# Kernel optimization log

Measured on AMD Instinct MI355X. Metric: run time of the kernel, lower is better.

The kernel has to match this reference:

```python
import jax, jax.numpy as jnp
import numpy as np

TEMPERATURE = 0.07
IGNORE_INDEX = -100
NEG_INF = -1e30


def setup_inputs() -> dict:
    key = jax.random.key(0)
    kg, ke, kl = jax.random.split(key, 3)
    B, P, H = 4, 4096, 256
    greek_embeds = jax.random.normal(kg, (B, P, H), dtype=jnp.float32)
    english_embeds = jax.random.normal(ke, (B, P, H), dtype=jnp.float32)
    # labels in {1 aligned, 0 not aligned, -100 ignore}, ~1/3 each
    raw = jax.random.randint(kl, (B, P), 0, 3)
    labels = jnp.where(raw == 2, IGNORE_INDEX, raw).astype(jnp.int32)
    return {"greek_embeds": greek_embeds, "english_embeds": english_embeds, "labels": labels}


def reference(greek_embeds, english_embeds, labels):
    # L2-normalize (F.normalize semantics: clamp norm at 1e-12)
    g = greek_embeds / jnp.clip(jnp.linalg.norm(greek_embeds, axis=-1, keepdims=True), 1e-12)
    e = english_embeds / jnp.clip(jnp.linalg.norm(english_embeds, axis=-1, keepdims=True), 1e-12)
    # [B, P, P] similarity
    sim = jnp.einsum("bph,bqh->bpq", g, e) / TEMPERATURE

    valid = labels != IGNORE_INDEX            # [B, P]
    pos = valid & (labels == 1)               # [B, P]
    neg = valid & (labels != 1)               # [B, P]
    # batch is processed only if >=2 valid pairs AND at least one pos AND one neg
    batch_ok = (valid.sum(-1) >= 2) & pos.any(-1) & neg.any(-1)  # [B]

    diag = jnp.diagonal(sim, axis1=1, axis2=2)                   # [B, P] positive logit
    neg_sims = jnp.where(neg[:, None, :], sim, NEG_INF)          # [B, P, P] negative logits
    # stable logsumexp over concat([diag_i], neg_sims_i)
    m = jnp.maximum(diag, neg_sims.max(-1))                      # [B, P]
    lse = m + jnp.log(jnp.exp(diag - m) + jnp.sum(jnp.exp(neg_sims - m[..., None]), -1))
    per_pos_loss = lse - diag                                    # cross_entropy with target=0

    mask = pos & batch_ok[:, None]
    count = mask.sum()
    total = jnp.sum(jnp.where(mask, per_pos_loss, 0.0))
    return jnp.where(count == 0, 0.0, total / count.astype(total.dtype))
```

## Files before the change

kernel.cpp:

```cpp
#include <hip/hip_runtime.h>
#include <hip/hip_bf16.h>
#include <math.h>

#define BB 4
#define PP 4096
#define HH 256
#define INV_T (1.0f/0.07f)
#define JSPLIT 8
#define NTILES (PP/16)
#define TILE_BYTES (16*HH*2)

typedef __attribute__((ext_vector_type(8))) short bf16x8;
typedef __attribute__((ext_vector_type(4))) float f32x4;

#define WAITVM(n) asm volatile("s_waitcnt vmcnt(" #n ")" ::: "memory")

__device__ __forceinline__ float waveReduceSum(float v){
  #pragma unroll
  for (int off = 32; off; off >>= 1) v += __shfl_xor(v, off);
  return v;
}

__device__ __forceinline__ unsigned short f2bf(float x){
  union { float f; unsigned u; } v; v.f = x;
  unsigned r = v.u + 0x7FFFu + ((v.u >> 16) & 1u);
  return (unsigned short)(r >> 16);
}

__device__ __forceinline__ void gload_lds16(const void* g, void* l){
  __builtin_amdgcn_global_load_lds(
      (const __attribute__((address_space(1))) unsigned int*)g,
      (__attribute__((address_space(3))) unsigned int*)l, 16, 0, 0);
}

__global__ void k_compact(const int* __restrict__ labels, int* __restrict__ meta,
                          int* __restrict__ posIdx, int* __restrict__ negIdx){
  int b = blockIdx.x;
  const int* lab = labels + b * PP;
  __shared__ int wP[4], wN[4], wV[4];
  __shared__ int basePos, baseNeg, baseVal;
  int tid = threadIdx.x, wave = tid >> 6, lane = tid & 63;
  if (tid == 0){ basePos = 0; baseNeg = 0; baseVal = 0; }
  __syncthreads();
  for (int c = 0; c < PP; c += 256){
    int p = c + tid;
    int l = lab[p];
    bool isP = (l == 1), isN = (l == 0), isV = (l != -100);
    unsigned long long bP = __ballot(isP), bN = __ballot(isN), bV = __ballot(isV);
    unsigned long long lt = (1ull << lane) - 1ull;
    if (lane == 0){ wP[wave] = __popcll(bP); wN[wave] = __popcll(bN); wV[wave] = __popcll(bV); }
    __syncthreads();
    int offP = 0, offN = 0;
    for (int w = 0; w < wave; w++){ offP += wP[w]; offN += wN[w]; }
    if (isP) posIdx[b*PP + basePos + offP + __popcll(bP & lt)] = p;
    if (isN) negIdx[b*PP + baseNeg + offN + __popcll(bN & lt)] = p;
    __syncthreads();
    if (tid == 0){
      basePos += wP[0] + wP[1] + wP[2] + wP[3];
      baseNeg += wN[0] + wN[1] + wN[2] + wN[3];
      baseVal += wV[0] + wV[1] + wV[2] + wV[3];
    }
    __syncthreads();
  }
  if (tid == 0){
    int Np = basePos, Nn = baseNeg, nv = baseVal;
    meta[b*4+0] = Np;
    meta[b*4+1] = Nn;
    meta[b*4+2] = (nv >= 2 && Np > 0 && Nn > 0) ? 1 : 0;
    meta[b*4+3] = nv;
  }
}

__global__ void k_norm(const float* __restrict__ greek, const float* __restrict__ english,
                       const int* __restrict__ meta, const int* __restrict__ posIdx,
                       const int* __restrict__ negIdx,
                       unsigned short* __restrict__ GposF, unsigned short* __restrict__ EnegF,
                       float* __restrict__ diag){
  int tid = threadIdx.x, wave = tid >> 6, lane = tid & 63;
  int gb = blockIdx.x;
  const int HALF = BB * PP / 4;
  bool isPos = gb < HALF;
  int rowBase = (gb % HALF) * 4 + wave;
  int b = rowBase / PP;
  int i = rowBase % PP;
  int Np = meta[b*4+0], Nn = meta[b*4+1];
  int Ncount = isPos ? Np : Nn;
  unsigned short* buf = isPos ? GposF : EnegF;
  char* dst = (char*)buf + ((size_t)b*NTILES + (i>>4))*TILE_BYTES
            + (lane>>3)*1024 + (((i&15) + ((lane>>1)&3)*16) << 4);

  if (i >= Ncount){
    if (i < ((Ncount + 15) & ~15) && !(lane & 1))
      *(uint4*)dst = make_uint4(0u,0u,0u,0u);
    return;
  }
  const int* idx = isPos ? posIdx : negIdx;
  int p = idx[b*PP + i];
  size_t base = ((size_t)b * PP + p) * HH + lane * 4;

  if (isPos){
    float4 g4 = *reinterpret_cast<const float4*>(greek + base);
    float ssg = waveReduceSum(g4.x*g4.x + g4.y*g4.y + g4.z*g4.z + g4.w*g4.w);
    float gs = 1.0f / fmaxf(sqrtf(ssg), 1e-12f);
    float gx = g4.x*gs, gy = g4.y*gs, gz = g4.z*gs, gw = g4.w*gs;
    unsigned u0 = (unsigned)f2bf(gx) | ((unsigned)f2bf(gy) << 16);
    unsigned u1 = (unsigned)f2bf(gz) | ((unsigned)f2bf(gw) << 16);
    unsigned o0 = __shfl_xor(u0, 1), o1 = __shfl_xor(u1, 1);
    if (!(lane & 1)) *(uint4*)dst = make_uint4(u0, u1, o0, o1);
    float4 e4 = *reinterpret_cast<const float4*>(english + base);
    float sse = waveReduceSum(e4.x*e4.x + e4.y*e4.y + e4.z*e4.z + e4.w*e4.w);
    float es = 1.0f / fmaxf(sqrtf(sse), 1e-12f);
    float d = waveReduceSum((gx*e4.x + gy*e4.y + gz*e4.z + gw*e4.w) * es);
    if (lane == 0) diag[b*PP + i] = d;
  } else {
    float4 e4 = *reinterpret_cast<const float4*>(english + base);
    float sse = waveReduceSum(e4.x*e4.x + e4.y*e4.y + e4.z*e4.z + e4.w*e4.w);
    float es = 1.0f / fmaxf(sqrtf(sse), 1e-12f);
    unsigned u0 = (unsigned)f2bf(e4.x*es) | ((unsigned)f2bf(e4.y*es) << 16);
    unsigned u1 = (unsigned)f2bf(e4.z*es) | ((unsigned)f2bf(e4.w*es) << 16);
    unsigned o0 = __shfl_xor(u0, 1), o1 = __shfl_xor(u1, 1);
    if (!(lane & 1)) *(uint4*)dst = make_uint4(u0, u1, o0, o1);
  }
}

__global__ void __launch_bounds__(256, 4)
k_loss(const unsigned short* __restrict__ GposF,
       const unsigned short* __restrict__ EnegF,
       const int* __restrict__ meta,
       float* __restrict__ Spart){
  int L = blockIdx.x;
  int rb = L >> 5;
  int pair = L & 31;
  int b = pair >> 3, chunk = pair & 7;
  int Np = meta[b*4+0], Nn = meta[b*4+1], ok = meta[b*4+2];
  int i0 = rb * 64;
  if (!ok || i0 >= Np) return;
  int tid = threadIdx.x, wave = tid >> 6, lane = tid & 63;
  int lo16 = lane & 15, hi4 = lane >> 4;
  int NT = (Nn + 15) >> 4;
  int TPC = (NT + JSPLIT - 1) / JSPLIT;
  int t0 = chunk * TPC, t1 = min(NT, t0 + TPC);

  __shared__ __align__(16) char Bs[3][TILE_BYTES];

  const char* AF = (const char*)GposF + ((size_t)b*NTILES + (i0 >> 4) + wave) * TILE_BYTES;
  bf16x8 a[8];
  #pragma unroll
  for (int kk = 0; kk < 8; kk++)
    a[kk] = *reinterpret_cast<const bf16x8*>(AF + kk*1024 + (lane << 4));

  const char* EF = (const char*)EnegF + (size_t)b * NTILES * TILE_BYTES;
  float s[4] = {0.f, 0.f, 0.f, 0.f};

  if (t0 < t1){
    {
      const char* src = EF + (size_t)t0*TILE_BYTES + (wave << 11) + (lane << 4);
      char* dstl = &Bs[0][wave << 11];
      gload_lds16(src, dstl);
      gload_lds16(src + 1024, dstl + 1024);
    }
    if (t0 + 1 < t1){
      const char* src = EF + (size_t)(t0+1)*TILE_BYTES + (wave << 11) + (lane << 4);
      char* dstl = &Bs[1][wave << 11];
      gload_lds16(src, dstl);
      gload_lds16(src + 1024, dstl + 1024);
    }
    int cur = 0;
    for (int t = t0; t < t1; t++){
      if (t + 1 < t1) WAITVM(2);
      else            WAITVM(0);
      __builtin_amdgcn_s_barrier();
      __builtin_amdgcn_sched_barrier(0);

      if (t + 2 < t1){
        int nb = cur + 2; if (nb >= 3) nb -= 3;
        const char* src = EF + (size_t)(t+2)*TILE_BYTES + (wave << 11) + (lane << 4);
        char* dstl = &Bs[nb][wave << 11];
        gload_lds16(src, dstl);
        gload_lds16(src + 1024, dstl + 1024);
      }

      const char* Bt = &Bs[cur][0];
      f32x4 c = {0.f, 0.f, 0.f, 0.f};
      #pragma unroll
      for (int kk = 0; kk < 8; kk++){
        bf16x8 bv = *reinterpret_cast<const bf16x8*>(Bt + kk*1024 + (lane << 4));
        c = __builtin_amdgcn_mfma_f32_16x16x32_bf16(a[kk], bv, c, 0, 0, 0);
      }
      bool cok = (t*16 + lo16) < Nn;
      #pragma unroll
      for (int r = 0; r < 4; r++)
        s[r] += cok ? __expf(c[r] * INV_T) : 0.0f;

      cur = (cur == 2) ? 0 : cur + 1;
    }
  }

  #pragma unroll
  for (int off = 1; off < 16; off <<= 1){
    #pragma unroll
    for (int r = 0; r < 4; r++) s[r] += __shfl_xor(s[r], off);
  }
  if (lo16 == 0){
    #pragma unroll
    for (int r = 0; r < 4; r++){
      int i = i0 + wave*16 + hi4*4 + r;
      Spart[(((size_t)b*PP + i) << 3) + chunk] = s[r];
    }
  }
}

__global__ void k_final(const float* __restrict__ Spart, const float* __restrict__ diag,
                        const int* __restrict__ meta, float* __restrict__ out){
  __shared__ float lds[16];
  int tid = threadIdx.x;
  int np[BB], okk[BB];
  #pragma unroll
  for (int b = 0; b < BB; b++){ np[b] = meta[b*4+0]; okk[b] = meta[b*4+2]; }
  float tot = 0.0f;
  for (int idx = tid; idx < BB*PP; idx += 1024){
    int b = idx >> 12, i = idx & (PP-1);
    if (!okk[b] || i >= np[b]) continue;
    const float4* p = reinterpret_cast<const float4*>(Spart + ((size_t)idx << 3));
    float4 p0 = p[0], p1 = p[1];
    float S = ((p0.x+p0.y)+(p0.z+p0.w)) + ((p1.x+p1.y)+(p1.z+p1.w));
    float dl = diag[idx] * INV_T;
    tot += logf(S + expf(dl)) - dl;
  }
  #pragma unroll
  for (int off = 32; off; off >>= 1) tot += __shfl_xor(tot, off);
  int wave = tid >> 6;
  if ((tid & 63) == 0) lds[wave] = tot;
  __syncthreads();
  if (tid == 0){
    float total = 0.0f;
    #pragma unroll
    for (int w = 0; w < 16; w++) total += lds[w];
    int count = 0;
    #pragma unroll
    for (int b = 0; b < BB; b++) if (okk[b]) count += np[b];
    out[0] = (count == 0) ? 0.0f : total / (float)count;
  }
}

extern "C" void kernel_launch(void* const* d_in, const int* in_sizes, int n_in,
                              void* d_out, int out_size, void* d_ws, size_t ws_size,
                              hipStream_t stream){
  const float* greek   = (const float*)d_in[0];
  const float* english = (const float*)d_in[1];
  const int*   labels  = (const int*)d_in[2];
  float* out = (float*)d_out;

  char* ws = (char*)d_ws;
  size_t off = 0;
  unsigned short* GposF = (unsigned short*)(ws + off); off += (size_t)BB*NTILES*TILE_BYTES;
  unsigned short* EnegF = (unsigned short*)(ws + off); off += (size_t)BB*NTILES*TILE_BYTES;
  float* Spart  = (float*)(ws + off); off += (size_t)BB*PP*JSPLIT*sizeof(float);
  float* diag   = (float*)(ws + off); off += (size_t)BB*PP*sizeof(float);
  int*   posIdx = (int*)(ws + off);   off += (size_t)BB*PP*sizeof(int);
  int*   negIdx = (int*)(ws + off);   off += (size_t)BB*PP*sizeof(int);
  int*   meta   = (int*)(ws + off);   off += 64;

  k_compact<<<BB, 256, 0, stream>>>(labels, meta, posIdx, negIdx);
  k_norm<<<2*BB*PP/4, 256, 0, stream>>>(greek, english, meta, posIdx, negIdx,
                                        GposF, EnegF, diag);
  k_loss<<<(PP/64)*32, 256, 0, stream>>>(GposF, EnegF, meta, Spart);
  k_final<<<1, 1024, 0, stream>>>(Spart, diag, meta, out);
}
```

Before: 42.19 us.

## Fuse prep kernels, mask negatives by bitmask, and fold final reduction into loss kernel

Merges label compaction and normalization into one prep kernel. Normalized rows are now written in natural row order instead of being gathered into compacted MFMA tiles. The loss kernel no longer works on a compacted negative set: it sweeps all columns and masks non-negatives with a per-batch bitmask. It then finishes the per-row logsumexp and the global mean with last-block atomic counters, which removes the separate final kernel. This cuts launches and the serial compaction-to-normalize dependency, but roughly triples the matmul and exp work in the loss kernel and adds atomics and fences.

```diff
diff --git a/kernel.cpp b/kernel.cpp
--- a/kernel.cpp
+++ b/kernel.cpp
@@ -6,20 +6,15 @@
 #define PP 4096
 #define HH 256
 #define INV_T (1.0f/0.07f)
-#define JSPLIT 8
-#define NTILES (PP/16)
-#define TILE_BYTES (16*HH*2)
+#define NRB 64
+#define TPC 32
+#define TILE_BYTES 8192
+#define D2GRID (NRB*32)
 
 typedef __attribute__((ext_vector_type(8))) short bf16x8;
 typedef __attribute__((ext_vector_type(4))) float f32x4;
 
 #define WAITVM(n) asm volatile("s_waitcnt vmcnt(" #n ")" ::: "memory")
-
-__device__ __forceinline__ float waveReduceSum(float v){
-  #pragma unroll
-  for (int off = 32; off; off >>= 1) v += __shfl_xor(v, off);
-  return v;
-}
 
 __device__ __forceinline__ unsigned short f2bf(float x){
   union { float f; unsigned u; } v; v.f = x;
@@ -33,213 +28,211 @@
       (__attribute__((address_space(3))) unsigned int*)l, 16, 0, 0);
 }
 
-__global__ void k_compact(const int* __restrict__ labels, int* __restrict__ meta,
-                          int* __restrict__ posIdx, int* __restrict__ negIdx){
-  int b = blockIdx.x;
-  const int* lab = labels + b * PP;
-  __shared__ int wP[4], wN[4], wV[4];
-  __shared__ int basePos, baseNeg, baseVal;
+__global__ void k_prep(const float* __restrict__ greek, const float* __restrict__ english,
+                       const int* __restrict__ labels,
+                       unsigned short* __restrict__ Gn, unsigned short* __restrict__ En,
+                       float* __restrict__ diagN, int* __restrict__ posIdx,
+                       int* __restrict__ meta, unsigned* __restrict__ negBits,
+                       int* __restrict__ ctrRB, float* __restrict__ partialTot,
+                       int* __restrict__ gctr){
   int tid = threadIdx.x, wave = tid >> 6, lane = tid & 63;
-  if (tid == 0){ basePos = 0; baseNeg = 0; baseVal = 0; }
-  __syncthreads();
-  for (int c = 0; c < PP; c += 256){
-    int p = c + tid;
-    int l = lab[p];
-    bool isP = (l == 1), isN = (l == 0), isV = (l != -100);
-    unsigned long long bP = __ballot(isP), bN = __ballot(isN), bV = __ballot(isV);
-    unsigned long long lt = (1ull << lane) - 1ull;
-    if (lane == 0){ wP[wave] = __popcll(bP); wN[wave] = __popcll(bN); wV[wave] = __popcll(bV); }
-    __syncthreads();
-    int offP = 0, offN = 0;
-    for (int w = 0; w < wave; w++){ offP += wP[w]; offN += wN[w]; }
-    if (isP) posIdx[b*PP + basePos + offP + __popcll(bP & lt)] = p;
-    if (isN) negIdx[b*PP + baseNeg + offN + __popcll(bN & lt)] = p;
-    __syncthreads();
+  if (blockIdx.x < BB){
+    int b = blockIdx.x;
+    if (tid < NRB){ ctrRB[b*NRB + tid] = 0; partialTot[b*NRB + tid] = 0.0f; }
+    if (b == 0 && tid == 64) gctr[0] = 0;
+    const int* lab = labels + b * PP;
+    __shared__ int wP[4], wN[4], wV[4];
+    __shared__ int basePos, baseNeg, baseVal;
+    if (tid == 0){ basePos = 0; baseNeg = 0; baseVal = 0; }
+    __syncthreads();
+    for (int c = 0; c < PP; c += 256){
+      int p = c + tid;
+      int l = lab[p];
+      bool isP = (l == 1), isN = (l == 0), isV = (l != -100);
+      unsigned long long bP = __ballot(isP), bN = __ballot(isN), bV = __ballot(isV);
+      unsigned long long lt = (1ull << lane) - 1ull;
+      if (lane == 0){
+        wP[wave] = __popcll(bP); wN[wave] = __popcll(bN); wV[wave] = __popcll(bV);
+        int w0 = (c + (wave << 6)) >> 5;
+        negBits[b*128 + w0]     = (unsigned)bN;
+        negBits[b*128 + w0 + 1] = (unsigned)(bN >> 32);
+      }
+      __syncthreads();
+      int offP = 0;
+      for (int w = 0; w < wave; w++) offP += wP[w];
+      if (isP) posIdx[b*PP + basePos + offP + __popcll(bP & lt)] = p;
+      __syncthreads();
+      if (tid == 0){
+        basePos += wP[0]+wP[1]+wP[2]+wP[3];
+        baseNeg += wN[0]+wN[1]+wN[2]+wN[3];
+        baseVal += wV[0]+wV[1]+wV[2]+wV[3];
+      }
+      __syncthreads();
+    }
     if (tid == 0){
-      basePos += wP[0] + wP[1] + wP[2] + wP[3];
-      baseNeg += wN[0] + wN[1] + wN[2] + wN[3];
-      baseVal += wV[0] + wV[1] + wV[2] + wV[3];
-    }
-    __syncthreads();
+      int Np = basePos, Nn = baseNeg, nv = baseVal;
+      meta[b*4+0] = Np; meta[b*4+1] = Nn;
+      meta[b*4+2] = (nv >= 2 && Np > 0 && Nn > 0) ? 1 : 0;
+      meta[b*4+3] = nv;
+    }
+  } else {
+    int u = (blockIdx.x - BB) * 4 + wave;
+    int lab = labels[u];
+    if (lab == -100) return;
+    size_t base = (size_t)u * HH + lane * 4;
+    if (lab == 1){
+      float4 g4 = *reinterpret_cast<const float4*>(greek + base);
+      float4 e4 = *reinterpret_cast<const float4*>(english + base);
+      float ag = g4.x*g4.x + g4.y*g4.y + g4.z*g4.z + g4.w*g4.w;
+      float ae = e4.x*e4.x + e4.y*e4.y + e4.z*e4.z + e4.w*e4.w;
+      float ad = g4.x*e4.x + g4.y*e4.y + g4.z*e4.z + g4.w*e4.w;
+      #pragma unroll
+      for (int off = 32; off; off >>= 1){
+        ag += __shfl_xor(ag, off); ae += __shfl_xor(ae, off); ad += __shfl_xor(ad, off);
+      }
+      float gs = 1.0f / fmaxf(sqrtf(ag), 1e-12f);
+      float es = 1.0f / fmaxf(sqrtf(ae), 1e-12f);
+      ushort4 go; go.x=f2bf(g4.x*gs); go.y=f2bf(g4.y*gs); go.z=f2bf(g4.z*gs); go.w=f2bf(g4.w*gs);
+      *reinterpret_cast<ushort4*>(Gn + (size_t)u*HH + lane*4) = go;
+      if (lane == 0) diagN[u] = ad * gs * es;
+    } else {
+      float4 e4 = *reinterpret_cast<const float4*>(english + base);
+      float ae = e4.x*e4.x + e4.y*e4.y + e4.z*e4.z + e4.w*e4.w;
+      #pragma unroll
+      for (int off = 32; off; off >>= 1) ae += __shfl_xor(ae, off);
+      float es = 1.0f / fmaxf(sqrtf(ae), 1e-12f);
+      ushort4 eo; eo.x=f2bf(e4.x*es); eo.y=f2bf(e4.y*es); eo.z=f2bf(e4.z*es); eo.w=f2bf(e4.w*es);
+      *reinterpret_cast<ushort4*>(En + (size_t)u*HH + lane*4) = eo;
+    }
   }
-  if (tid == 0){
-    int Np = basePos, Nn = baseNeg, nv = baseVal;
-    meta[b*4+0] = Np;
-    meta[b*4+1] = Nn;
-    meta[b*4+2] = (nv >= 2 && Np > 0 && Nn > 0) ? 1 : 0;
-    meta[b*4+3] = nv;
-  }
-}
-
-__global__ void k_norm(const float* __restrict__ greek, const float* __restrict__ english,
-                       const int* __restrict__ meta, const int* __restrict__ posIdx,
-                       const int* __restrict__ negIdx,
-                       unsigned short* __restrict__ GposF, unsigned short* __restrict__ EnegF,
-                       float* __restrict__ diag){
-  int tid = threadIdx.x, wave = tid >> 6, lane = tid & 63;
-  int gb = blockIdx.x;
-  const int HALF = BB * PP / 4;
-  bool isPos = gb < HALF;
-  int rowBase = (gb % HALF) * 4 + wave;
-  int b = rowBase / PP;
-  int i = rowBase % PP;
-  int Np = meta[b*4+0], Nn = meta[b*4+1];
-  int Ncount = isPos ? Np : Nn;
-  unsigned short* buf = isPos ? GposF : EnegF;
-  char* dst = (char*)buf + ((size_t)b*NTILES + (i>>4))*TILE_BYTES
-            + (lane>>3)*1024 + (((i&15) + ((lane>>1)&3)*16) << 4);
-
-  if (i >= Ncount){
-    if (i < ((Ncount + 15) & ~15) && !(lane & 1))
-      *(uint4*)dst = make_uint4(0u,0u,0u,0u);
-    return;
-  }
-  const int* idx = isPos ? posIdx : negIdx;
-  int p = idx[b*PP + i];
-  size_t base = ((size_t)b * PP + p) * HH + lane * 4;
-
-  if (isPos){
-    float4 g4 = *reinterpret_cast<const float4*>(greek + base);
-    float ssg = waveReduceSum(g4.x*g4.x + g4.y*g4.y + g4.z*g4.z + g4.w*g4.w);
-    float gs = 1.0f / fmaxf(sqrtf(ssg), 1e-12f);
-    float gx = g4.x*gs, gy = g4.y*gs, gz = g4.z*gs, gw = g4.w*gs;
-    unsigned u0 = (unsigned)f2bf(gx) | ((unsigned)f2bf(gy) << 16);
-    unsigned u1 = (unsigned)f2bf(gz) | ((unsigned)f2bf(gw) << 16);
-    unsigned o0 = __shfl_xor(u0, 1), o1 = __shfl_xor(u1, 1);
-    if (!(lane & 1)) *(uint4*)dst = make_uint4(u0, u1, o0, o1);
-    float4 e4 = *reinterpret_cast<const float4*>(english + base);
-    float sse = waveReduceSum(e4.x*e4.x + e4.y*e4.y + e4.z*e4.z + e4.w*e4.w);
-    float es = 1.0f / fmaxf(sqrtf(sse), 1e-12f);
-    float d = waveReduceSum((gx*e4.x + gy*e4.y + gz*e4.z + gw*e4.w) * es);
-    if (lane == 0) diag[b*PP + i] = d;
-  } else {
-    float4 e4 = *reinterpret_cast<const float4*>(english + base);
-    float sse = waveReduceSum(e4.x*e4.x + e4.y*e4.y + e4.z*e4.z + e4.w*e4.w);
-    float es = 1.0f / fmaxf(sqrtf(sse), 1e-12f);
-    unsigned u0 = (unsigned)f2bf(e4.x*es) | ((unsigned)f2bf(e4.y*es) << 16);
-    unsigned u1 = (unsigned)f2bf(e4.z*es) | ((unsigned)f2bf(e4.w*es) << 16);
-    unsigned o0 = __shfl_xor(u0, 1), o1 = __shfl_xor(u1, 1);
-    if (!(lane & 1)) *(uint4*)dst = make_uint4(u0, u1, o0, o1);
-  }
 }
 
 __global__ void __launch_bounds__(256, 4)
-k_loss(const unsigned short* __restrict__ GposF,
-       const unsigned short* __restrict__ EnegF,
-       const int* __restrict__ meta,
-       float* __restrict__ Spart){
+k_loss(const unsigned short* __restrict__ Gn, const unsigned short* __restrict__ En,
+       const float* __restrict__ diagN, const int* __restrict__ posIdx,
+       const int* __restrict__ meta, const unsigned* __restrict__ negBits,
+       float* __restrict__ Spart, int* __restrict__ ctrRB,
+       float* __restrict__ partialTot, int* __restrict__ gctr,
+       float* __restrict__ out){
   int L = blockIdx.x;
-  int rb = L >> 5;
-  int pair = L & 31;
-  int b = pair >> 3, chunk = pair & 7;
-  int Np = meta[b*4+0], Nn = meta[b*4+1], ok = meta[b*4+2];
-  int i0 = rb * 64;
-  if (!ok || i0 >= Np) return;
+  int rb = L >> 5, b = (L >> 3) & 3, chunk = L & 7;
   int tid = threadIdx.x, wave = tid >> 6, lane = tid & 63;
   int lo16 = lane & 15, hi4 = lane >> 4;
-  int NT = (Nn + 15) >> 4;
-  int TPC = (NT + JSPLIT - 1) / JSPLIT;
-  int t0 = chunk * TPC, t1 = min(NT, t0 + TPC);
+  int Np = meta[b*4+0], ok = meta[b*4+2];
+  int i0 = rb * 64;
+  bool active = ok && (i0 < Np);
 
   __shared__ __align__(16) char Bs[3][TILE_BYTES];
-
-  const char* AF = (const char*)GposF + ((size_t)b*NTILES + (i0 >> 4) + wave) * TILE_BYTES;
-  bf16x8 a[8];
-  #pragma unroll
-  for (int kk = 0; kk < 8; kk++)
-    a[kk] = *reinterpret_cast<const bf16x8*>(AF + kk*1024 + (lane << 4));
-
-  const char* EF = (const char*)EnegF + (size_t)b * NTILES * TILE_BYTES;
-  float s[4] = {0.f, 0.f, 0.f, 0.f};
-
-  if (t0 < t1){
-    {
-      const char* src = EF + (size_t)t0*TILE_BYTES + (wave << 11) + (lane << 4);
-      char* dstl = &Bs[0][wave << 11];
-      gload_lds16(src, dstl);
-      gload_lds16(src + 1024, dstl + 1024);
-    }
-    if (t0 + 1 < t1){
-      const char* src = EF + (size_t)(t0+1)*TILE_BYTES + (wave << 11) + (lane << 4);
-      char* dstl = &Bs[1][wave << 11];
-      gload_lds16(src, dstl);
-      gload_lds16(src + 1024, dstl + 1024);
-    }
+  __shared__ unsigned nb16[16];
+  __shared__ int shI;
+  __shared__ float shF[4];
+
+  if (active){
+    if (tid < 16) nb16[tid] = negBits[b*128 + chunk*16 + tid];
+
+    int iw = i0 + wave*16;
+    int ii = min(iw + lo16, Np-1);
+    int prow = posIdx[b*PP + ii];
+    const char* Ab = (const char*)Gn + ((size_t)b*PP + prow)*(HH*2) + hi4*16;
+    bf16x8 a[8];
+    #pragma unroll
+    for (int kk = 0; kk < 8; kk++)
+      a[kk] = *reinterpret_cast<const bf16x8*>(Ab + kk*64);
+
+    const char* Eb = (const char*)En + (size_t)b*PP*(HH*2);
+    int T0 = chunk * TPC;
+    __syncthreads();
+
+    auto STAGE = [&](int t, int buf){
+      size_t cb = (size_t)(t*16 + lo16)*(HH*2) + hi4*16;
+      char* d = &Bs[buf][wave << 11];
+      gload_lds16(Eb + cb + (size_t)(2*wave+0)*64, d);
+      gload_lds16(Eb + cb + (size_t)(2*wave+1)*64, d + 1024);
+    };
+    STAGE(T0, 0);
+    STAGE(T0+1, 1);
+
+    float s[4] = {0.f,0.f,0.f,0.f};
     int cur = 0;
-    for (int t = t0; t < t1; t++){
-      if (t + 1 < t1) WAITVM(2);
-      else            WAITVM(0);
+    for (int t = T0; t < T0 + TPC; t++){
+      if (t + 1 < T0 + TPC) WAITVM(2);
+      else                  WAITVM(0);
       __builtin_amdgcn_s_barrier();
       __builtin_amdgcn_sched_barrier(0);
-
-      if (t + 2 < t1){
-        int nb = cur + 2; if (nb >= 3) nb -= 3;
-        const char* src = EF + (size_t)(t+2)*TILE_BYTES + (wave << 11) + (lane << 4);
-        char* dstl = &Bs[nb][wave << 11];
-        gload_lds16(src, dstl);
-        gload_lds16(src + 1024, dstl + 1024);
-      }
-
+      if (t + 2 < T0 + TPC){
+        int nbuf = cur + 2; if (nbuf >= 3) nbuf -= 3;
+        STAGE(t+2, nbuf);
+      }
       const char* Bt = &Bs[cur][0];
-      f32x4 c = {0.f, 0.f, 0.f, 0.f};
+      f32x4 c = {0.f,0.f,0.f,0.f};
       #pragma unroll
       for (int kk = 0; kk < 8; kk++){
         bf16x8 bv = *reinterpret_cast<const bf16x8*>(Bt + kk*1024 + (lane << 4));
         c = __builtin_amdgcn_mfma_f32_16x16x32_bf16(a[kk], bv, c, 0, 0, 0);
       }
-      bool cok = (t*16 + lo16) < Nn;
+      unsigned mw = nb16[(t >> 1) - chunk*16];
+      bool cok = (mw >> (lo16 + ((t & 1) << 4))) & 1;
       #pragma unroll
       for (int r = 0; r < 4; r++)
         s[r] += cok ? __expf(c[r] * INV_T) : 0.0f;
-
       cur = (cur == 2) ? 0 : cur + 1;
     }
+
+    #pragma unroll
+    for (int off = 1; off < 16; off <<= 1){
+      #pragma unroll
+      for (int r = 0; r < 4; r++) s[r] += __shfl_xor(s[r], off);
+    }
+    if (lo16 == 0){
+      #pragma unroll
+      for (int r = 0; r < 4; r++){
+        int i = iw + hi4*4 + r;
+        Spart[(((size_t)b*PP + i) << 3) + chunk] = s[r];
+      }
+    }
+
+    __threadfence();
+    if (tid == 0) shI = atomicAdd(&ctrRB[b*NRB + rb], 1);
+    __syncthreads();
+    if (shI == 7){
+      __threadfence();
+      if (tid < 64){
+        float v = 0.0f;
+        int i = i0 + tid;
+        if (i < Np){
+          const float4* p4 = reinterpret_cast<const float4*>(Spart + (((size_t)b*PP + i) << 3));
+          float4 p0 = p4[0], p1 = p4[1];
+          float S = ((p0.x+p0.y)+(p0.z+p0.w)) + ((p1.x+p1.y)+(p1.z+p1.w));
+          float dl = diagN[b*PP + posIdx[b*PP + i]] * INV_T;
+          v = logf(S + __expf(dl)) - dl;
+        }
+        #pragma unroll
+        for (int off = 32; off; off >>= 1) v += __shfl_xor(v, off);
+        if (tid == 0) partialTot[b*NRB + rb] = v;
+      }
+      __threadfence();
+    }
   }
 
-  #pragma unroll
-  for (int off = 1; off < 16; off <<= 1){
+  __syncthreads();
+  if (tid == 0) shI = atomicAdd(gctr, 1);
+  __syncthreads();
+  if (shI == D2GRID - 1){
+    __threadfence();
+    float v = 0.0f;
+    int b2 = tid >> 6;
+    if (meta[b2*4+2]) v = partialTot[tid];
     #pragma unroll
-    for (int r = 0; r < 4; r++) s[r] += __shfl_xor(s[r], off);
-  }
-  if (lo16 == 0){
-    #pragma unroll
-    for (int r = 0; r < 4; r++){
-      int i = i0 + wave*16 + hi4*4 + r;
-      Spart[(((size_t)b*PP + i) << 3) + chunk] = s[r];
-    }
-  }
-}
-
-__global__ void k_final(const float* __restrict__ Spart, const float* __restrict__ diag,
-                        const int* __restrict__ meta, float* __restrict__ out){
-  __shared__ float lds[16];
-  int tid = threadIdx.x;
-  int np[BB], okk[BB];
-  #pragma unroll
-  for (int b = 0; b < BB; b++){ np[b] = meta[b*4+0]; okk[b] = meta[b*4+2]; }
-  float tot = 0.0f;
-  for (int idx = tid; idx < BB*PP; idx += 1024){
-    int b = idx >> 12, i = idx & (PP-1);
-    if (!okk[b] || i >= np[b]) continue;
-    const float4* p = reinterpret_cast<const float4*>(Spart + ((size_t)idx << 3));
-    float4 p0 = p[0], p1 = p[1];
-    float S = ((p0.x+p0.y)+(p0.z+p0.w)) + ((p1.x+p1.y)+(p1.z+p1.w));
-    float dl = diag[idx] * INV_T;
-    tot += logf(S + expf(dl)) - dl;
-  }
-  #pragma unroll
-  for (int off = 32; off; off >>= 1) tot += __shfl_xor(tot, off);
-  int wave = tid >> 6;
-  if ((tid & 63) == 0) lds[wave] = tot;
-  __syncthreads();
-  if (tid == 0){
-    float total = 0.0f;
-    #pragma unroll
-    for (int w = 0; w < 16; w++) total += lds[w];
-    int count = 0;
-    #pragma unroll
-    for (int b = 0; b < BB; b++) if (okk[b]) count += np[b];
-    out[0] = (count == 0) ? 0.0f : total / (float)count;
+    for (int off = 32; off; off >>= 1) v += __shfl_xor(v, off);
+    if (lane == 0) shF[wave] = v;
+    __syncthreads();
+    if (tid == 0){
+      float total = shF[0] + shF[1] + shF[2] + shF[3];
+      int count = 0;
+      #pragma unroll
+      for (int bb = 0; bb < BB; bb++) if (meta[bb*4+2]) count += meta[bb*4+0];
+      out[0] = (count == 0) ? 0.0f : total / (float)count;
+    }
   }
 }
 
@@ -253,17 +246,19 @@
 
   char* ws = (char*)d_ws;
   size_t off = 0;
-  unsigned short* GposF = (unsigned short*)(ws + off); off += (size_t)BB*NTILES*TILE_BYTES;
-  unsigned short* EnegF = (unsigned short*)(ws + off); off += (size_t)BB*NTILES*TILE_BYTES;
-  float* Spart  = (float*)(ws + off); off += (size_t)BB*PP*JSPLIT*sizeof(float);
-  float* diag   = (float*)(ws + off); off += (size_t)BB*PP*sizeof(float);
-  int*   posIdx = (int*)(ws + off);   off += (size_t)BB*PP*sizeof(int);
-  int*   negIdx = (int*)(ws + off);   off += (size_t)BB*PP*sizeof(int);
-  int*   meta   = (int*)(ws + off);   off += 64;
-
-  k_compact<<<BB, 256, 0, stream>>>(labels, meta, posIdx, negIdx);
-  k_norm<<<2*BB*PP/4, 256, 0, stream>>>(greek, english, meta, posIdx, negIdx,
-                                        GposF, EnegF, diag);
-  k_loss<<<(PP/64)*32, 256, 0, stream>>>(GposF, EnegF, meta, Spart);
-  k_final<<<1, 1024, 0, stream>>>(Spart, diag, meta, out);
-}
+  unsigned short* Gn   = (unsigned short*)(ws + off); off += (size_t)BB*PP*HH*2;
+  unsigned short* En   = (unsigned short*)(ws + off); off += (size_t)BB*PP*HH*2;
+  float* Spart      = (float*)(ws + off); off += (size_t)BB*PP*8*sizeof(float);
+  float* diagN      = (float*)(ws + off); off += (size_t)BB*PP*sizeof(float);
+  int*   posIdx     = (int*)(ws + off);   off += (size_t)BB*PP*sizeof(int);
+  int*   meta       = (int*)(ws + off);   off += 64;
+  unsigned* negBits = (unsigned*)(ws + off); off += (size_t)BB*128*sizeof(unsigned);
+  int*   ctrRB      = (int*)(ws + off);   off += (size_t)BB*NRB*sizeof(int);
+  float* partialTot = (float*)(ws + off); off += (size_t)BB*NRB*sizeof(float);
+  int*   gctr       = (int*)(ws + off);   off += 64;
+
+  k_prep<<<BB + BB*PP/4, 256, 0, stream>>>(greek, english, labels, Gn, En, diagN,
+                                           posIdx, meta, negBits, ctrRB, partialTot, gctr);
+  k_loss<<<D2GRID, 256, 0, stream>>>(Gn, En, diagN, posIdx, meta, negBits,
+                                     Spart, ctrRB, partialTot, gctr, out);
+}
```

After: 158.1 us. 3.75x slower.

## Replace index compaction with rank scan and scatter-based normalization

Applied to the files above, without the earlier changes.

The label compaction kernel becomes a two-pass scan. It counts per-wave positives and negatives across all chunks, builds prefix offsets once, and writes a per-element rank instead of gathered index lists. The normalization kernel now walks the original rows, with each wave covering one row index across all batches, and scatters normalized bf16 tiles to the rank slot. It fuses the three wave reductions into a single shuffle loop, which removes the indirect gather and cuts the grid size. The explicit zero-fill of tail padding rows is dropped, so correctness depends on the loss kernel masking out-of-range columns. The final exp also switches to the fast intrinsic.

```diff
diff --git a/kernel.cpp b/kernel.cpp
--- a/kernel.cpp
+++ b/kernel.cpp
@@ -8,18 +8,12 @@
 #define INV_T (1.0f/0.07f)
 #define JSPLIT 8
 #define NTILES (PP/16)
-#define TILE_BYTES (16*HH*2)
+#define TILE_BYTES 8192
 
 typedef __attribute__((ext_vector_type(8))) short bf16x8;
 typedef __attribute__((ext_vector_type(4))) float f32x4;
 
 #define WAITVM(n) asm volatile("s_waitcnt vmcnt(" #n ")" ::: "memory")
-
-__device__ __forceinline__ float waveReduceSum(float v){
-  #pragma unroll
-  for (int off = 32; off; off >>= 1) v += __shfl_xor(v, off);
-  return v;
-}
 
 __device__ __forceinline__ unsigned short f2bf(float x){
   union { float f; unsigned u; } v; v.f = x;
@@ -33,93 +27,96 @@
       (__attribute__((address_space(3))) unsigned int*)l, 16, 0, 0);
 }
 
-__global__ void k_compact(const int* __restrict__ labels, int* __restrict__ meta,
-                          int* __restrict__ posIdx, int* __restrict__ negIdx){
+__global__ void k_scan(const int* __restrict__ labels, int* __restrict__ meta,
+                       int* __restrict__ rank){
   int b = blockIdx.x;
   const int* lab = labels + b * PP;
-  __shared__ int wP[4], wN[4], wV[4];
-  __shared__ int basePos, baseNeg, baseVal;
   int tid = threadIdx.x, wave = tid >> 6, lane = tid & 63;
-  if (tid == 0){ basePos = 0; baseNeg = 0; baseVal = 0; }
+  __shared__ int cP[64], cN[64];
+  __shared__ int pP[65], pN[65];
+  __shared__ int vtot[4];
+  int myLab[16];
+  int vcnt = 0;
+  #pragma unroll
+  for (int c = 0; c < 16; c++){
+    int l = lab[c*256 + tid];
+    myLab[c] = l;
+    unsigned long long bP = __ballot(l == 1), bN = __ballot(l == 0);
+    vcnt += (l != -100) ? 1 : 0;
+    if (lane == 0){ cP[c*4 + wave] = __popcll(bP); cN[c*4 + wave] = __popcll(bN); }
+  }
+  #pragma unroll
+  for (int off = 32; off; off >>= 1) vcnt += __shfl_xor(vcnt, off);
+  if (lane == 0) vtot[wave] = vcnt;
   __syncthreads();
-  for (int c = 0; c < PP; c += 256){
-    int p = c + tid;
-    int l = lab[p];
-    bool isP = (l == 1), isN = (l == 0), isV = (l != -100);
-    unsigned long long bP = __ballot(isP), bN = __ballot(isN), bV = __ballot(isV);
+  if (tid < 64){
+    int sp = 0, sn = 0;
+    for (int k = 0; k < tid; k++){ sp += cP[k]; sn += cN[k]; }
+    pP[tid] = sp; pN[tid] = sn;
+    if (tid == 63){ pP[64] = sp + cP[63]; pN[64] = sn + cN[63]; }
+  }
+  __syncthreads();
+  #pragma unroll
+  for (int c = 0; c < 16; c++){
+    int l = myLab[c];
+    unsigned long long bP = __ballot(l == 1), bN = __ballot(l == 0);
     unsigned long long lt = (1ull << lane) - 1ull;
-    if (lane == 0){ wP[wave] = __popcll(bP); wN[wave] = __popcll(bN); wV[wave] = __popcll(bV); }
-    __syncthreads();
-    int offP = 0, offN = 0;
-    for (int w = 0; w < wave; w++){ offP += wP[w]; offN += wN[w]; }
-    if (isP) posIdx[b*PP + basePos + offP + __popcll(bP & lt)] = p;
-    if (isN) negIdx[b*PP + baseNeg + offN + __popcll(bN & lt)] = p;
-    __syncthreads();
-    if (tid == 0){
-      basePos += wP[0] + wP[1] + wP[2] + wP[3];
-      baseNeg += wN[0] + wN[1] + wN[2] + wN[3];
-      baseVal += wV[0] + wV[1] + wV[2] + wV[3];
-    }
-    __syncthreads();
+    int p = b*PP + c*256 + tid;
+    if (l == 1)      rank[p] = pP[c*4 + wave] + __popcll(bP & lt);
+    else if (l == 0) rank[p] = pN[c*4 + wave] + __popcll(bN & lt);
   }
   if (tid == 0){
-    int Np = basePos, Nn = baseNeg, nv = baseVal;
-    meta[b*4+0] = Np;
-    meta[b*4+1] = Nn;
+    int Np = pP[64], Nn = pN[64], nv = vtot[0]+vtot[1]+vtot[2]+vtot[3];
+    meta[b*4+0] = Np; meta[b*4+1] = Nn;
     meta[b*4+2] = (nv >= 2 && Np > 0 && Nn > 0) ? 1 : 0;
     meta[b*4+3] = nv;
   }
 }
 
 __global__ void k_norm(const float* __restrict__ greek, const float* __restrict__ english,
-                       const int* __restrict__ meta, const int* __restrict__ posIdx,
-                       const int* __restrict__ negIdx,
+                       const int* __restrict__ labels, const int* __restrict__ rank,
                        unsigned short* __restrict__ GposF, unsigned short* __restrict__ EnegF,
-                       float* __restrict__ diag){
+                       float* __restrict__ diagC){
   int tid = threadIdx.x, wave = tid >> 6, lane = tid & 63;
-  int gb = blockIdx.x;
-  const int HALF = BB * PP / 4;
-  bool isPos = gb < HALF;
-  int rowBase = (gb % HALF) * 4 + wave;
-  int b = rowBase / PP;
-  int i = rowBase % PP;
-  int Np = meta[b*4+0], Nn = meta[b*4+1];
-  int Ncount = isPos ? Np : Nn;
-  unsigned short* buf = isPos ? GposF : EnegF;
-  char* dst = (char*)buf + ((size_t)b*NTILES + (i>>4))*TILE_BYTES
-            + (lane>>3)*1024 + (((i&15) + ((lane>>1)&3)*16) << 4);
-
-  if (i >= Ncount){
-    if (i < ((Ncount + 15) & ~15) && !(lane & 1))
-      *(uint4*)dst = make_uint4(0u,0u,0u,0u);
-    return;
-  }
-  const int* idx = isPos ? posIdx : negIdx;
-  int p = idx[b*PP + i];
-  size_t base = ((size_t)b * PP + p) * HH + lane * 4;
-
-  if (isPos){
-    float4 g4 = *reinterpret_cast<const float4*>(greek + base);
-    float ssg = waveReduceSum(g4.x*g4.x + g4.y*g4.y + g4.z*g4.z + g4.w*g4.w);
-    float gs = 1.0f / fmaxf(sqrtf(ssg), 1e-12f);
-    float gx = g4.x*gs, gy = g4.y*gs, gz = g4.z*gs, gw = g4.w*gs;
-    unsigned u0 = (unsigned)f2bf(gx) | ((unsigned)f2bf(gy) << 16);
-    unsigned u1 = (unsigned)f2bf(gz) | ((unsigned)f2bf(gw) << 16);
-    unsigned o0 = __shfl_xor(u0, 1), o1 = __shfl_xor(u1, 1);
-    if (!(lane & 1)) *(uint4*)dst = make_uint4(u0, u1, o0, o1);
-    float4 e4 = *reinterpret_cast<const float4*>(english + base);
-    float sse = waveReduceSum(e4.x*e4.x + e4.y*e4.y + e4.z*e4.z + e4.w*e4.w);
-    float es = 1.0f / fmaxf(sqrtf(sse), 1e-12f);
-    float d = waveReduceSum((gx*e4.x + gy*e4.y + gz*e4.z + gw*e4.w) * es);
-    if (lane == 0) diag[b*PP + i] = d;
-  } else {
-    float4 e4 = *reinterpret_cast<const float4*>(english + base);
-    float sse = waveReduceSum(e4.x*e4.x + e4.y*e4.y + e4.z*e4.z + e4.w*e4.w);
-    float es = 1.0f / fmaxf(sqrtf(sse), 1e-12f);
-    unsigned u0 = (unsigned)f2bf(e4.x*es) | ((unsigned)f2bf(e4.y*es) << 16);
-    unsigned u1 = (unsigned)f2bf(e4.z*es) | ((unsigned)f2bf(e4.w*es) << 16);
-    unsigned o0 = __shfl_xor(u0, 1), o1 = __shfl_xor(u1, 1);
-    if (!(lane & 1)) *(uint4*)dst = make_uint4(u0, u1, o0, o1);
+  int r0 = blockIdx.x * 4 + wave;
+  for (int b = 0; b < BB; b++){
+    int u = b * PP + r0;
+    int lab = labels[u];
+    if (lab == -100) continue;
+    size_t base = (size_t)u * HH + lane * 4;
+    int rk = rank[u];
+    if (lab == 1){
+      float4 g4 = *reinterpret_cast<const float4*>(greek + base);
+      float4 e4 = *reinterpret_cast<const float4*>(english + base);
+      float ag = g4.x*g4.x + g4.y*g4.y + g4.z*g4.z + g4.w*g4.w;
+      float ae = e4.x*e4.x + e4.y*e4.y + e4.z*e4.z + e4.w*e4.w;
+      float ad = g4.x*e4.x + g4.y*e4.y + g4.z*e4.z + g4.w*e4.w;
+      #pragma unroll
+      for (int off = 32; off; off >>= 1){
+        ag += __shfl_xor(ag, off); ae += __shfl_xor(ae, off); ad += __shfl_xor(ad, off);
+      }
+      float gs = 1.0f / fmaxf(sqrtf(ag), 1e-12f);
+      float es = 1.0f / fmaxf(sqrtf(ae), 1e-12f);
+      unsigned u0 = (unsigned)f2bf(g4.x*gs) | ((unsigned)f2bf(g4.y*gs) << 16);
+      unsigned u1 = (unsigned)f2bf(g4.z*gs) | ((unsigned)f2bf(g4.w*gs) << 16);
+      unsigned o0 = __shfl_xor(u0, 1), o1 = __shfl_xor(u1, 1);
+      char* dst = (char*)GposF + ((size_t)b*NTILES + (rk>>4))*TILE_BYTES
+                + (lane>>3)*1024 + (((rk&15) + ((lane>>1)&3)*16) << 4);
+      if (!(lane & 1)) *(uint4*)dst = make_uint4(u0, u1, o0, o1);
+      if (lane == 0) diagC[b*PP + rk] = ad * gs * es;
+    } else {
+      float4 e4 = *reinterpret_cast<const float4*>(english + base);
+      float ae = e4.x*e4.x + e4.y*e4.y + e4.z*e4.z + e4.w*e4.w;
+      #pragma unroll
+      for (int off = 32; off; off >>= 1) ae += __shfl_xor(ae, off);
+      float es = 1.0f / fmaxf(sqrtf(ae), 1e-12f);
+      unsigned u0 = (unsigned)f2bf(e4.x*es) | ((unsigned)f2bf(e4.y*es) << 16);
+      unsigned u1 = (unsigned)f2bf(e4.z*es) | ((unsigned)f2bf(e4.w*es) << 16);
+      unsigned o0 = __shfl_xor(u0, 1), o1 = __shfl_xor(u1, 1);
+      char* dst = (char*)EnegF + ((size_t)b*NTILES + (rk>>4))*TILE_BYTES
+                + (lane>>3)*1024 + (((rk&15) + ((lane>>1)&3)*16) << 4);
+      if (!(lane & 1)) *(uint4*)dst = make_uint4(u0, u1, o0, o1);
+    }
   }
 }
 
@@ -210,7 +207,7 @@
   }
 }
 
-__global__ void k_final(const float* __restrict__ Spart, const float* __restrict__ diag,
+__global__ void k_final(const float* __restrict__ Spart, const float* __restrict__ diagC,
                         const int* __restrict__ meta, float* __restrict__ out){
   __shared__ float lds[16];
   int tid = threadIdx.x;
@@ -224,8 +221,8 @@
     const float4* p = reinterpret_cast<const float4*>(Spart + ((size_t)idx << 3));
     float4 p0 = p[0], p1 = p[1];
     float S = ((p0.x+p0.y)+(p0.z+p0.w)) + ((p1.x+p1.y)+(p1.z+p1.w));
-    float dl = diag[idx] * INV_T;
-    tot += logf(S + expf(dl)) - dl;
+    float dl = diagC[idx] * INV_T;
+    tot += logf(S + __expf(dl)) - dl;
   }
   #pragma unroll
   for (int off = 32; off; off >>= 1) tot += __shfl_xor(tot, off);
@@ -255,15 +252,13 @@
   size_t off = 0;
   unsigned short* GposF = (unsigned short*)(ws + off); off += (size_t)BB*NTILES*TILE_BYTES;
   unsigned short* EnegF = (unsigned short*)(ws + off); off += (size_t)BB*NTILES*TILE_BYTES;
-  float* Spart  = (float*)(ws + off); off += (size_t)BB*PP*JSPLIT*sizeof(float);
-  float* diag   = (float*)(ws + off); off += (size_t)BB*PP*sizeof(float);
-  int*   posIdx = (int*)(ws + off);   off += (size_t)BB*PP*sizeof(int);
-  int*   negIdx = (int*)(ws + off);   off += (size_t)BB*PP*sizeof(int);
+  float* Spart  = (float*)(ws + off); off += (size_t)BB*PP*8*sizeof(float);
+  float* diagC  = (float*)(ws + off); off += (size_t)BB*PP*sizeof(float);
+  int*   rank   = (int*)(ws + off);   off += (size_t)BB*PP*sizeof(int);
   int*   meta   = (int*)(ws + off);   off += 64;
 
-  k_compact<<<BB, 256, 0, stream>>>(labels, meta, posIdx, negIdx);
-  k_norm<<<2*BB*PP/4, 256, 0, stream>>>(greek, english, meta, posIdx, negIdx,
-                                        GposF, EnegF, diag);
+  k_scan<<<BB, 256, 0, stream>>>(labels, meta, rank);
+  k_norm<<<PP/4, 256, 0, stream>>>(greek, english, labels, rank, GposF, EnegF, diagC);
   k_loss<<<(PP/64)*32, 256, 0, stream>>>(GposF, EnegF, meta, Spart);
-  k_final<<<1, 1024, 0, stream>>>(Spart, diag, meta, out);
-}
+  k_final<<<1, 1024, 0, stream>>>(Spart, diagC, meta, out);
+}
```

Measured after the change: 39.36 us. 6.7% less time.
